# Optimization experiments

Hardware: AMD Instinct MI355X
Metric: run time of the kernel (lower is better)

Reference implementation:

```python
import jax, jax.numpy as jnp
import numpy as np

N_NODES = 100000
N_EDGES = 600000
N_GRAPHS = 128
IN_DIM = 4
HID = 32
HEADS1 = 4
NEG_SLOPE = 0.2


def _segment_softmax(e, seg, n):
    # e: [E, H], softmax over edges sharing the same destination node
    m = jax.ops.segment_max(e, seg, num_segments=n)
    ex = jnp.exp(e - m[seg])
    s = jax.ops.segment_sum(ex, seg, num_segments=n)
    return ex / s[seg]


def _gat_layer(x, src, dst, W, a_src, a_dst, b, heads, ch):
    # PyG GATConv: h = x W (per-head), alpha = softmax_dst(leaky_relu(a_s.h_src + a_d.h_dst))
    n = x.shape[0]
    h = (x @ W).reshape(n, heads, ch)                       # [N, H, C]
    al_s = jnp.einsum('nhc,hc->nh', h, a_src)               # [N, H]
    al_d = jnp.einsum('nhc,hc->nh', h, a_dst)
    e = jax.nn.leaky_relu(al_s[src] + al_d[dst], NEG_SLOPE)  # [E, H]
    alpha = _segment_softmax(e, dst, n)                      # [E, H]
    msg = h[src] * alpha[:, :, None]                         # [E, H, C]
    out = jax.ops.segment_sum(msg, dst, num_segments=n)     # [N, H, C]
    return out.reshape(n, heads * ch) + b


def setup_inputs() -> dict:
    key = jax.random.key(0)
    ks = jax.random.split(key, 16)
    s = 0.1
    return {
        'x': jax.random.normal(ks[0], (N_NODES, IN_DIM), jnp.float32),
        'edge_index': jax.random.randint(ks[1], (2, N_EDGES), 0, N_NODES, jnp.int64),
        'batch': jax.random.randint(ks[2], (N_NODES,), 0, N_GRAPHS, jnp.int64),
        'W1': jax.random.normal(ks[3], (IN_DIM, HEADS1 * HID), jnp.float32) * s,
        'a_s1': jax.random.normal(ks[4], (HEADS1, HID), jnp.float32) * s,
        'a_d1': jax.random.normal(ks[5], (HEADS1, HID), jnp.float32) * s,
        'b1': jnp.zeros((HEADS1 * HID,), jnp.float32),
        'W2': jax.random.normal(ks[6], (HEADS1 * HID, HID), jnp.float32) * s,
        'a_s2': jax.random.normal(ks[7], (1, HID), jnp.float32) * s,
        'a_d2': jax.random.normal(ks[8], (1, HID), jnp.float32) * s,
        'b2': jnp.zeros((HID,), jnp.float32),
        'Wc1': jax.random.normal(ks[9], (HID, 32), jnp.float32) * s,
        'bc1': jnp.zeros((32,), jnp.float32),
        'Wc2': jax.random.normal(ks[10], (32, 1), jnp.float32) * s,
        'bc2': jnp.zeros((1,), jnp.float32),
    }


def reference(x, edge_index, batch, W1, a_s1, a_d1, b1, W2, a_s2, a_d2, b2, Wc1, bc1, Wc2, bc2):
    n = x.shape[0]
    loops = jnp.arange(n, dtype=edge_index.dtype)
    src = jnp.concatenate([edge_index[0], loops])   # add_self_loops=True (PyG default)
    dst = jnp.concatenate([edge_index[1], loops])
    h = jax.nn.elu(_gat_layer(x, src, dst, W1, a_s1, a_d1, b1, HEADS1, HID))
    h = jax.nn.elu(_gat_layer(h, src, dst, W2, a_s2, a_d2, b2, 1, HID))
    # global_mean_pool
    sums = jax.ops.segment_sum(h, batch, num_segments=N_GRAPHS)
    cnt = jax.ops.segment_sum(jnp.ones((n, 1), h.dtype), batch, num_segments=N_GRAPHS)
    g = sums / jnp.maximum(cnt, 1.0)
    z = jax.nn.relu(g @ Wc1 + bc1)
    return jax.nn.sigmoid(z @ Wc2 + bc2)
```

## Files before the change

### kernel.cpp

```cpp
#include <hip/hip_runtime.h>
#include <hip/hip_fp16.h>
#include <float.h>

#define NEG 0.2f
#define NPART 16
#define PAD 32

typedef _Float16 half8 __attribute__((ext_vector_type(8)));
typedef float f32x4 __attribute__((ext_vector_type(4)));

__device__ __forceinline__ float lrelu(float x){ return x > 0.f ? x : NEG * x; }
__device__ __forceinline__ float elu1(float x){ return x > 0.f ? x : (__expf(x) - 1.f); }

__global__ void k_scat(const int* __restrict__ ei, const int* __restrict__ batch,
                       int* __restrict__ cur, int* __restrict__ csr_src,
                       float* __restrict__ gcnt, int N, int E){
  __shared__ float gc[128];
  int tid = threadIdx.x;
  bool doh = blockIdx.x < 256;
  if (doh && tid < 128) gc[tid] = 0.f;
  __syncthreads();
  int idx = blockIdx.x * 256 + tid;
  int gstr = gridDim.x * 256;
  for (int e = idx; e < E; e += gstr){
    int s = ei[e], d = ei[E + e];
    int pos = atomicAdd(cur + d, 1);
    if (pos < PAD) csr_src[(size_t)d * PAD + pos] = s;
  }
  if (doh){
    for (int n = idx; n < N; n += 256 * 256)
      atomicAdd(&gc[batch[n]], 1.f);
    __syncthreads();
    if (tid < 128 && gc[tid] != 0.f) atomicAdd(gcnt + tid, gc[tid]);
  }
}

__global__ void __launch_bounds__(256, 6)
k_layer1(const int* __restrict__ degp, const int* __restrict__ csr_src,
         const float* __restrict__ x, const float* __restrict__ W1,
         const float* __restrict__ as1, const float* __restrict__ ad1,
         const float* __restrict__ b1, const float* __restrict__ W2,
         const float* __restrict__ as2, const float* __restrict__ ad2,
         __half* __restrict__ h2h, float* __restrict__ als2,
         float* __restrict__ ald2, int N){
  __shared__ float PQ[2][16];
  __shared__ __align__(16) float xa[32][20];
  __shared__ __align__(16) _Float16 out1sh[32][136];
  __shared__ __align__(16) float h2sh[32][36];
  __shared__ float als_s[32], ald_s[32];
  int tid = threadIdx.x;
  const float4* x4 = (const float4*)x;

  int g1 = tid >> 3, l = tid & 7;
  int node1 = blockIdx.x * 32 + g1;
  int nd = node1 < N ? node1 : N - 1;
  int deg = degp[nd];
  size_t r0 = (size_t)nd * PAD;
  int s_pre = csr_src[r0 + l];
  int total = (node1 < N) ? deg + 1 : 0;
  int s0 = (l < deg) ? s_pre : nd;
  float4 xv0 = x4[s0];
  float4 xn = x4[nd];

  if (tid < 32){
    int which = tid >> 4, kh = tid & 15, k = kh >> 2, h = kh & 3;
    const float* a = which ? ad1 : as1;
    float s = 0.f;
    #pragma unroll 8
    for (int c = 0; c < 32; c++) s += W1[k*128 + h*32 + c] * a[h*32 + c];
    PQ[which][kh] = s;
  }
  __syncthreads();

  {
    float P[16], Q[16];
    #pragma unroll
    for (int i = 0; i < 16; i++){ P[i] = PQ[0][i]; Q[i] = PQ[1][i]; }
    float ald0 = xn.x*Q[0] + xn.y*Q[4] + xn.z*Q[8]  + xn.w*Q[12];
    float ald1_ = xn.x*Q[1] + xn.y*Q[5] + xn.z*Q[9]  + xn.w*Q[13];
    float ald2_ = xn.x*Q[2] + xn.y*Q[6] + xn.z*Q[10] + xn.w*Q[14];
    float ald3 = xn.x*Q[3] + xn.y*Q[7] + xn.z*Q[11] + xn.w*Q[15];
    float acc[16];
    #pragma unroll
    for (int i = 0; i < 16; i++) acc[i] = 0.f;
    float ss[4] = {0.f, 0.f, 0.f, 0.f};
    if (l < total){
      float4 xv = xv0;
      float a0 = xv.x*P[0] + xv.y*P[4] + xv.z*P[8]  + xv.w*P[12];
      float a1 = xv.x*P[1] + xv.y*P[5] + xv.z*P[9]  + xv.w*P[13];
      float a2 = xv.x*P[2] + xv.y*P[6] + xv.z*P[10] + xv.w*P[14];
      float a3 = xv.x*P[3] + xv.y*P[7] + xv.z*P[11] + xv.w*P[15];
      float e0 = __expf(lrelu(a0 + ald0));
      float e1 = __expf(lrelu(a1 + ald1_));
      float e2 = __expf(lrelu(a2 + ald2_));
      float e3 = __expf(lrelu(a3 + ald3));
      ss[0] += e0; ss[1] += e1; ss[2] += e2; ss[3] += e3;
      acc[0]  += e0*xv.x; acc[1]  += e0*xv.y; acc[2]  += e0*xv.z; acc[3]  += e0*xv.w;
      acc[4]  += e1*xv.x; acc[5]  += e1*xv.y; acc[6]  += e1*xv.z; acc[7]  += e1*xv.w;
      acc[8]  += e2*xv.x; acc[9]  += e2*xv.y; acc[10] += e2*xv.z; acc[11] += e2*xv.w;
      acc[12] += e3*xv.x; acc[13] += e3*xv.y; acc[14] += e3*xv.z; acc[15] += e3*xv.w;
    }
    for (int t = l + 8; t < total; t += 8){
      int s = (t < deg) ? csr_src[r0 + t] : nd;
      float4 xv = x4[s];
      float a0 = xv.x*P[0] + xv.y*P[4] + xv.z*P[8]  + xv.w*P[12];
      float a1 = xv.x*P[1] + xv.y*P[5] + xv.z*P[9]  + xv.w*P[13];
      float a2 = xv.x*P[2] + xv.y*P[6] + xv.z*P[10] + xv.w*P[14];
      float a3 = xv.x*P[3] + xv.y*P[7] + xv.z*P[11] + xv.w*P[15];
      float e0 = __expf(lrelu(a0 + ald0));
      float e1 = __expf(lrelu(a1 + ald1_));
      float e2 = __expf(lrelu(a2 + ald2_));
      float e3 = __expf(lrelu(a3 + ald3));
      ss[0] += e0; ss[1] += e1; ss[2] += e2; ss[3] += e3;
      acc[0]  += e0*xv.x; acc[1]  += e0*xv.y; acc[2]  += e0*xv.z; acc[3]  += e0*xv.w;
      acc[4]  += e1*xv.x; acc[5]  += e1*xv.y; acc[6]  += e1*xv.z; acc[7]  += e1*xv.w;
      acc[8]  += e2*xv.x; acc[9]  += e2*xv.y; acc[10] += e2*xv.z; acc[11] += e2*xv.w;
      acc[12] += e3*xv.x; acc[13] += e3*xv.y; acc[14] += e3*xv.z; acc[15] += e3*xv.w;
    }
    #pragma unroll
    for (int m = 4; m >= 1; m >>= 1){
      #pragma unroll
      for (int i = 0; i < 16; i++) acc[i] += __shfl_xor(acc[i], m, 8);
      #pragma unroll
      for (int i = 0; i < 4; i++)  ss[i]  += __shfl_xor(ss[i], m, 8);
    }
    if (l == 0){
      float* o = xa[g1];
      *(float4*)(o)      = make_float4(acc[0],  acc[1],  acc[2],  acc[3]);
      *(float4*)(o + 4)  = make_float4(acc[4],  acc[5],  acc[6],  acc[7]);
      *(float4*)(o + 8)  = make_float4(acc[8],  acc[9],  acc[10], acc[11]);
      *(float4*)(o + 12) = make_float4(acc[12], acc[13], acc[14], acc[15]);
      *(float4*)(o + 16) = make_float4(ss[0], ss[1], ss[2], ss[3]);
    }
  }
  __syncthreads();
  if (tid < 128) xa[tid >> 2][16 + (tid & 3)] = 1.f / xa[tid >> 2][16 + (tid & 3)];
  __builtin_amdgcn_sched_barrier(0);

  int wv = tid >> 6, lane = tid & 63;
  int wm = wv >> 1, wn = wv & 1;
  int lrow = lane & 15, lk8 = lane >> 4;
  half8 bf[4];
  #pragma unroll
  for (int t = 0; t < 4; t++){
    #pragma unroll
    for (int j = 0; j < 8; j++)
      bf[t][j] = (_Float16)W2[(t*32 + lk8*8 + j)*32 + wn*16 + lrow];
  }
  int c128 = ((wv & 1) << 6) | lane;
  int gbase = (wv >> 1) << 4;
  int hh = c128 >> 5;
  float w1c0 = W1[c128], w1c1 = W1[128 + c128];
  float w1c2 = W1[256 + c128], w1c3 = W1[384 + c128];
  float b1c = b1[c128];
  __syncthreads();

  #pragma unroll
  for (int i = 0; i < 16; i++){
    int g = gbase + i;
    const float* xg = xa[g];
    float4 xv = *(const float4*)(xg + hh*4);
    float rs = xg[16 + hh];
    float o = elu1((xv.x*w1c0 + xv.y*w1c1 + xv.z*w1c2 + xv.w*w1c3) * rs + b1c);
    out1sh[g][c128] = (_Float16)o;
  }
  __syncthreads();

  {
    f32x4 acc2 = {0.f, 0.f, 0.f, 0.f};
    #pragma unroll
    for (int t = 0; t < 4; t++){
      half8 af = *(const half8*)(&out1sh[wm*16 + lrow][t*32 + lk8*8]);
      acc2 = __builtin_amdgcn_mfma_f32_16x16x32_f16(af, bf[t], acc2, 0, 0, 0);
    }
    #pragma unroll
    for (int i = 0; i < 4; i++)
      h2sh[wm*16 + lk8*4 + i][wn*16 + lrow] = acc2[i];
  }
  __syncthreads();

  {
    int g = tid >> 3, q = tid & 7;
    int node = blockIdx.x * 32 + g;
    float4 hv = *(const float4*)(&h2sh[g][q*4]);
    if (node < N){
      __half2 pa = __floats2half2_rn(hv.x, hv.y);
      __half2 pb = __floats2half2_rn(hv.z, hv.w);
      __half2* dst = (__half2*)(h2h + (size_t)node*32 + q*4);
      dst[0] = pa; dst[1] = pb;
    }
    float4 sa = *(const float4*)(as2 + q*4);
    float4 da = *(const float4*)(ad2 + q*4);
    float ps = hv.x*sa.x + hv.y*sa.y + hv.z*sa.z + hv.w*sa.w;
    float pd = hv.x*da.x + hv.y*da.y + hv.z*da.z + hv.w*da.w;
    #pragma unroll
    for (int m = 4; m >= 1; m >>= 1){
      ps += __shfl_xor(ps, m, 8);
      pd += __shfl_xor(pd, m, 8);
    }
    if (q == 0){ als_s[g] = ps; ald_s[g] = pd; }
  }
  __syncthreads();
  if (tid < 32){
    int node = blockIdx.x * 32 + tid;
    if (node < N){ als2[node] = als_s[tid]; ald2[node] = ald_s[tid]; }
  }
}

__global__ void __launch_bounds__(256)
k_gat2(const int* __restrict__ degp, const int* __restrict__ csr_src,
       const __half* __restrict__ h2h, const float* __restrict__ als2,
       const float* __restrict__ ald2, const float* __restrict__ b2,
       const int* __restrict__ batch, float* __restrict__ gsum_part, int N){
  int tid = threadIdx.x;
  int node = blockIdx.x * 32 + (tid >> 3);
  if (node >= N) return;
  int l = tid & 7;
  int deg = degp[node];
  size_t r0 = (size_t)node * PAD;
  int total = deg + 1;
  float ald = ald2[node];
  float4 b2v = *(const float4*)(b2 + (l << 2));

  float ssum = 0.f;
  float f0 = 0.f, f1 = 0.f, f2 = 0.f, f3 = 0.f;
  for (int base = 0; base < total; base += 8){
    int t = base + l;
    int s = (t < deg) ? csr_src[r0 + t] : node;
    float ex = (t < total) ? __expf(lrelu(als2[s] + ald)) : 0.f;
    ssum += ex;
    #pragma unroll
    for (int j = 0; j < 8; j++){
      float ej = __shfl(ex, j, 8);
      int   sj = __shfl(s,  j, 8);
      union { float2 f; __half2 h[2]; } u;
      u.f = *(const float2*)(h2h + (size_t)sj*32 + (l << 2));
      float2 v0 = __half22float2(u.h[0]), v1 = __half22float2(u.h[1]);
      f0 += ej*v0.x; f1 += ej*v0.y; f2 += ej*v1.x; f3 += ej*v1.y;
    }
  }
  ssum += __shfl_xor(ssum, 1, 8);
  ssum += __shfl_xor(ssum, 2, 8);
  ssum += __shfl_xor(ssum, 4, 8);
  float rs = 1.f / ssum;
  int b = batch[node];
  float* gp = gsum_part + ((blockIdx.x & (NPART-1)) << 12) + b*32 + (l << 2);
  atomicAdd(gp + 0, elu1(f0*rs + b2v.x));
  atomicAdd(gp + 1, elu1(f1*rs + b2v.y));
  atomicAdd(gp + 2, elu1(f2*rs + b2v.z));
  atomicAdd(gp + 3, elu1(f3*rs + b2v.w));
}

__global__ void k_head(const float* __restrict__ gsum_part, const float* __restrict__ gcnt,
                       const float* __restrict__ Wc1, const float* __restrict__ bc1,
                       const float* __restrict__ Wc2, const float* __restrict__ bc2,
                       float* __restrict__ out){
  int g = blockIdx.x, tid = threadIdx.x;
  __shared__ float gl[32];
  if (tid < 32){
    float s = 0.f;
    #pragma unroll
    for (int p = 0; p < NPART; p++) s += gsum_part[(p << 12) + g*32 + tid];
    float cnt = gcnt[g];
    cnt = cnt > 1.f ? cnt : 1.f;
    gl[tid] = s / cnt;
  }
  __syncthreads();
  if (tid < 32){
    float z = bc1[tid];
    #pragma unroll 8
    for (int c2 = 0; c2 < 32; c2++) z += gl[c2] * Wc1[c2*32 + tid];
    z = z > 0.f ? z : 0.f;
    float r = z * Wc2[tid];
    #pragma unroll
    for (int m = 16; m >= 1; m >>= 1) r += __shfl_xor(r, m, 32);
    if (tid == 0) out[g] = 1.f / (1.f + expf(-(r + bc2[0])));
  }
}

extern "C" void kernel_launch(void* const* d_in, const int* in_sizes, int n_in,
                              void* d_out, int out_size, void* d_ws, size_t ws_size,
                              hipStream_t stream){
  const float* x   = (const float*)d_in[0];
  const int*   ei  = (const int*)d_in[1];
  const int*   bat = (const int*)d_in[2];
  const float* W1  = (const float*)d_in[3];
  const float* as1 = (const float*)d_in[4];
  const float* ad1 = (const float*)d_in[5];
  const float* b1  = (const float*)d_in[6];
  const float* W2  = (const float*)d_in[7];
  const float* as2 = (const float*)d_in[8];
  const float* ad2 = (const float*)d_in[9];
  const float* b2  = (const float*)d_in[10];
  const float* Wc1 = (const float*)d_in[11];
  const float* bc1 = (const float*)d_in[12];
  const float* Wc2 = (const float*)d_in[13];
  const float* bc2 = (const float*)d_in[14];
  float* out = (float*)d_out;

  const int N = in_sizes[2];
  const int E = in_sizes[1] / 2;

  float* ws = (float*)d_ws;
  size_t off = 0;
  int* cur    = (int*)ws;           off += (size_t)N;
  float* gsum_part = ws + off;      off += (size_t)NPART * 4096;
  float* gcnt = ws + off;           off += 128;
  const size_t zero_elems = off;
  __half* h2h = (__half*)(ws + off); off += (size_t)N * 16;
  float* als2 = ws + off;           off += (size_t)N;
  float* ald2 = ws + off;           off += (size_t)N;
  int* csr_src= (int*)(ws + off);   off += (size_t)N * PAD;

  hipMemsetAsync(d_ws, 0, zero_elems * sizeof(float), stream);

  k_scat<<<(E + 255) / 256, 256, 0, stream>>>(ei, bat, cur, csr_src, gcnt, N, E);

  k_layer1<<<(N + 31) / 32, 256, 0, stream>>>(cur, csr_src, x, W1, as1, ad1, b1,
                                              W2, as2, ad2, h2h, als2, ald2, N);

  k_gat2<<<(N + 31) / 32, 256, 0, stream>>>(cur, csr_src, h2h, als2, ald2, b2,
                                            bat, gsum_part, N);

  k_head<<<128, 64, 0, stream>>>(gsum_part, gcnt, Wc1, bc1, Wc2, bc2, out);
}
```

Baseline: 199.9 us.

## Use 16 lanes per node in GAT layer-2 aggregation with split edge halves

The layer-2 aggregation kernel now gives each destination node 16 lanes instead of 8. The two 8-lane halves each take alternate edges, four neighbour rows at a time, with independent loads, and the partial sums are combined by a cross-half shuffle at the end. Each lane then writes two channels through atomics instead of four. The aim is more memory-level parallelism and a shorter loop for nodes with about seven incoming edges, at the cost of twice as many threads and extra shuffles.

```diff
diff --git a/kernel.cpp b/kernel.cpp
--- a/kernel.cpp
+++ b/kernel.cpp
@@ -213,42 +213,60 @@
        const float* __restrict__ ald2, const float* __restrict__ b2,
        const int* __restrict__ batch, float* __restrict__ gsum_part, int N){
   int tid = threadIdx.x;
-  int node = blockIdx.x * 32 + (tid >> 3);
+  int node = blockIdx.x * 16 + (tid >> 4);
   if (node >= N) return;
-  int l = tid & 7;
+  int l = tid & 15;
+  int sub = l >> 3;
+  int c4 = l & 7;
   int deg = degp[node];
   size_t r0 = (size_t)node * PAD;
   int total = deg + 1;
   float ald = ald2[node];
-  float4 b2v = *(const float4*)(b2 + (l << 2));
 
   float ssum = 0.f;
   float f0 = 0.f, f1 = 0.f, f2 = 0.f, f3 = 0.f;
-  for (int base = 0; base < total; base += 8){
+  for (int base = 0; base < total; base += 16){
     int t = base + l;
     int s = (t < deg) ? csr_src[r0 + t] : node;
     float ex = (t < total) ? __expf(lrelu(als2[s] + ald)) : 0.f;
     ssum += ex;
-    #pragma unroll
-    for (int j = 0; j < 8; j++){
-      float ej = __shfl(ex, j, 8);
-      int   sj = __shfl(s,  j, 8);
-      union { float2 f; __half2 h[2]; } u;
-      u.f = *(const float2*)(h2h + (size_t)sj*32 + (l << 2));
-      float2 v0 = __half22float2(u.h[0]), v1 = __half22float2(u.h[1]);
-      f0 += ej*v0.x; f1 += ej*v0.y; f2 += ej*v1.x; f3 += ej*v1.y;
-    }
-  }
-  ssum += __shfl_xor(ssum, 1, 8);
-  ssum += __shfl_xor(ssum, 2, 8);
-  ssum += __shfl_xor(ssum, 4, 8);
+    int lim = min(16, total - base);
+    for (int jj = 0; jj < lim; jj += 8){
+      int ja = jj + sub, jb = jj + 2 + sub, jc = jj + 4 + sub, jd = jj + 6 + sub;
+      float ea = __shfl(ex, ja, 16); int sa = __shfl(s, ja, 16);
+      float eb = __shfl(ex, jb, 16); int sb = __shfl(s, jb, 16);
+      float ec = __shfl(ex, jc, 16); int sc = __shfl(s, jc, 16);
+      float ed = __shfl(ex, jd, 16); int sd = __shfl(s, jd, 16);
+      union { float2 f; __half2 h[2]; } ua, ub, uc, ud;
+      ua.f = *(const float2*)(h2h + (size_t)sa*32 + (c4 << 2));
+      ub.f = *(const float2*)(h2h + (size_t)sb*32 + (c4 << 2));
+      uc.f = *(const float2*)(h2h + (size_t)sc*32 + (c4 << 2));
+      ud.f = *(const float2*)(h2h + (size_t)sd*32 + (c4 << 2));
+      float2 va0 = __half22float2(ua.h[0]), va1 = __half22float2(ua.h[1]);
+      float2 vb0 = __half22float2(ub.h[0]), vb1 = __half22float2(ub.h[1]);
+      float2 vc0 = __half22float2(uc.h[0]), vc1 = __half22float2(uc.h[1]);
+      float2 vd0 = __half22float2(ud.h[0]), vd1 = __half22float2(ud.h[1]);
+      f0 += ea*va0.x + eb*vb0.x + ec*vc0.x + ed*vd0.x;
+      f1 += ea*va0.y + eb*vb0.y + ec*vc0.y + ed*vd0.y;
+      f2 += ea*va1.x + eb*vb1.x + ec*vc1.x + ed*vd1.x;
+      f3 += ea*va1.y + eb*vb1.y + ec*vc1.y + ed*vd1.y;
+    }
+  }
+  f0 += __shfl_xor(f0, 8, 16);
+  f1 += __shfl_xor(f1, 8, 16);
+  f2 += __shfl_xor(f2, 8, 16);
+  f3 += __shfl_xor(f3, 8, 16);
+  #pragma unroll
+  for (int m = 8; m >= 1; m >>= 1) ssum += __shfl_xor(ssum, m, 16);
   float rs = 1.f / ssum;
+  float va = sub ? f2 : f0;
+  float vb = sub ? f3 : f1;
+  int ch = (c4 << 2) + (sub << 1);
+  float2 b2v = *(const float2*)(b2 + ch);
   int b = batch[node];
-  float* gp = gsum_part + ((blockIdx.x & (NPART-1)) << 12) + b*32 + (l << 2);
-  atomicAdd(gp + 0, elu1(f0*rs + b2v.x));
-  atomicAdd(gp + 1, elu1(f1*rs + b2v.y));
-  atomicAdd(gp + 2, elu1(f2*rs + b2v.z));
-  atomicAdd(gp + 3, elu1(f3*rs + b2v.w));
+  float* gp = gsum_part + ((blockIdx.x & (NPART-1)) << 12) + b*32 + ch;
+  atomicAdd(gp + 0, elu1(va*rs + b2v.x));
+  atomicAdd(gp + 1, elu1(vb*rs + b2v.y));
 }
 
 __global__ void k_head(const float* __restrict__ gsum_part, const float* __restrict__ gcnt,
@@ -319,7 +337,7 @@
   k_layer1<<<(N + 31) / 32, 256, 0, stream>>>(cur, csr_src, x, W1, as1, ad1, b1,
                                               W2, as2, ad2, h2h, als2, ald2, N);
 
-  k_gat2<<<(N + 31) / 32, 256, 0, stream>>>(cur, csr_src, h2h, als2, ald2, b2,
+  k_gat2<<<(N + 15) / 16, 256, 0, stream>>>(cur, csr_src, h2h, als2, ald2, b2,
                                             bat, gsum_part, N);
 
   k_head<<<128, 64, 0, stream>>>(gsum_part, gcnt, Wc1, bc1, Wc2, bc2, out);
```

After: 176.7 us. -11.6%, faster.
